# Performance work log

Hardware: AMD Instinct MI355X
Metric: run time of the kernel (lower is better)

## Reference

```python
import jax, jax.numpy as jnp
import numpy as np

N_BASIS = 128   # n_atom_basis F
N_INT   = 3     # n_interactions
N_RBF   = 20
CUTOFF  = 5.0
MAX_Z   = 100
EPS     = 1e-8
N_ATOMS = 25000
N_EDGES = 200000


def setup_inputs() -> dict:
    key = jax.random.key(0)
    ks = jax.random.split(key, 16)
    F = N_BASIS
    s = 0.02
    z     = jax.random.randint(ks[0], (N_ATOMS,), 1, MAX_Z)
    pos   = jax.random.uniform(ks[1], (N_ATOMS, 3), dtype=jnp.float32) * 2.0  # small box -> inside cutoff
    idx_i = jax.random.randint(ks[2], (N_EDGES,), 0, N_ATOMS)
    idx_j = jax.random.randint(ks[3], (N_EDGES,), 0, N_ATOMS)
    emb   = jax.random.normal(ks[4], (MAX_Z, F), dtype=jnp.float32) * s
    fW    = jax.random.normal(ks[5], (N_RBF, 3 * F * N_INT), dtype=jnp.float32) * s
    fb    = jnp.zeros((3 * F * N_INT,), jnp.float32)
    iW1   = jax.random.normal(ks[6], (N_INT, F, F), dtype=jnp.float32) * s
    ib1   = jnp.zeros((N_INT, F), jnp.float32)
    iW2   = jax.random.normal(ks[7], (N_INT, F, 3 * F), dtype=jnp.float32) * s
    ib2   = jnp.zeros((N_INT, 3 * F), jnp.float32)
    mWmix = jax.random.normal(ks[8], (N_INT, F, 2 * F), dtype=jnp.float32) * s
    mW1   = jax.random.normal(ks[9], (N_INT, 2 * F, F), dtype=jnp.float32) * s
    mb1   = jnp.zeros((N_INT, F), jnp.float32)
    mW2   = jax.random.normal(ks[10], (N_INT, F, 3 * F), dtype=jnp.float32) * s
    mb2   = jnp.zeros((N_INT, 3 * F), jnp.float32)
    return dict(z=z, pos=pos, idx_i=idx_i, idx_j=idx_j, emb=emb, fW=fW, fb=fb,
                iW1=iW1, ib1=ib1, iW2=iW2, ib2=ib2,
                mWmix=mWmix, mW1=mW1, mb1=mb1, mW2=mW2, mb2=mb2)


def reference(z, pos, idx_i, idx_j, emb, fW, fb, iW1, ib1, iW2, ib2,
              mWmix, mW1, mb1, mW2, mb2):
    F = N_BASIS
    n_atoms = z.shape[0]
    # geometry
    r_ij = pos[idx_j] - pos[idx_i]                                  # [E,3]
    r_ij = jnp.where(jnp.abs(r_ij) < 1e-6, 1e-6, r_ij)
    d_ij = jnp.linalg.norm(r_ij, axis=1, keepdims=True)             # [E,1]
    dir_ij = r_ij / d_ij                                            # [E,3]
    # Gaussian radial basis
    offsets = jnp.linspace(0.0, CUTOFF, N_RBF)
    width = offsets[1] - offsets[0]
    coeff = -0.5 / (width * width)
    phi = jnp.exp(coeff * (d_ij[..., None] - offsets) ** 2)         # [E,1,n_rbf]
    # cosine cutoff
    fcut = 0.5 * (jnp.cos(jnp.pi * d_ij / CUTOFF) + 1.0) * (d_ij < CUTOFF)  # [E,1]
    filters = (phi @ fW + fb) * fcut[..., None]                     # [E,1,3F*I]
    filter_list = jnp.split(filters, N_INT, axis=-1)                # each [E,1,3F]
    # initial atom features
    q = emb[z][:, None, :]                                          # [N,1,F]
    mu = jnp.zeros((n_atoms, 3, F), q.dtype)                        # [N,3,F]
    for t in range(N_INT):
        # --- interaction (gather - filter-multiply - scatter-add) ---
        x = jax.nn.silu(q @ iW1[t] + ib1[t]) @ iW2[t] + ib2[t]      # [N,1,3F]
        xj = x[idx_j]                                               # [E,1,3F]
        muj = mu[idx_j]                                             # [E,3,F]
        x = filter_list[t] * xj                                     # [E,1,3F]
        dq, dmuR, dmumu = jnp.split(x, 3, axis=-1)                  # [E,1,F] each
        dq = jax.ops.segment_sum(dq, idx_i, num_segments=n_atoms)   # [N,1,F]
        dmu = dmuR * dir_ij[..., None] + dmumu * muj                # [E,3,F]
        dmu = jax.ops.segment_sum(dmu, idx_i, num_segments=n_atoms) # [N,3,F]
        q = q + dq
        mu = mu + dmu
        # --- mixing (intra-atomic) ---
        mu_mix = mu @ mWmix[t]                                      # [N,3,2F]
        mu_V, mu_W = jnp.split(mu_mix, 2, axis=-1)                  # [N,3,F]
        mu_Vn = jnp.sqrt(jnp.sum(mu_V ** 2, axis=-2, keepdims=True) + EPS)  # [N,1,F]
        ctx = jnp.concatenate([q, mu_Vn], axis=-1)                  # [N,1,2F]
        x = jax.nn.silu(ctx @ mW1[t] + mb1[t]) @ mW2[t] + mb2[t]    # [N,1,3F]
        dq_intra, dmu_intra, dqmu_intra = jnp.split(x, 3, axis=-1)
        dmu_intra = dmu_intra * mu_W                                # [N,3,F]
        dqmu_intra = dqmu_intra * jnp.sum(mu_V * mu_W, axis=1, keepdims=True)
        q = q + dq_intra + dqmu_intra
        mu = mu + dmu_intra
    return q.squeeze(1), mu
```

## Files before the change

kernel.cpp:

```cpp
#include <hip/hip_runtime.h>
#include <hip/hip_bf16.h>

#define F 128
#define F3 384
#define NRBF 20
#define NITER 3
#define KP 24

typedef __hip_bfloat16 bf16;
typedef __bf16 bfrag __attribute__((ext_vector_type(8)));
typedef float f32x4 __attribute__((ext_vector_type(4)));

__device__ __forceinline__ float b2f(bf16 v) { return __bfloat162float(v); }
__device__ __forceinline__ bf16 f2b(float v) { return __float2bfloat16(v); }
__device__ __forceinline__ bfrag ldb(const bf16* p) { return *(const bfrag*)p; }
__device__ __forceinline__ bfrag ldsb(const __bf16* p) { return *(const bfrag*)p; }
__device__ __forceinline__ bfrag cvtf(const float* p) {
    bfrag r;
#pragma unroll
    for (int j = 0; j < 8; ++j) r[j] = (__bf16)p[j];
    return r;
}

__global__ void detect_kernel(const unsigned short* __restrict__ raw, int n_u16,
                              int* __restrict__ flag) {
    int i = blockIdx.x * blockDim.x + threadIdx.x;
    int bad = 0;
    for (int k = i; k < n_u16; k += blockDim.x * gridDim.x) {
        unsigned e = (raw[k] >> 7) & 0xFFu;
        if (e >= 140u) bad = 1;
    }
    if (bad) atomicOr(flag, 1);
}

struct CvtArgs {
    const void* src[13];
    float* dst[13];
    int end[14];
};
__global__ void cvt_all_kernel(CvtArgs a, const int* __restrict__ flag, int total) {
    int idx = blockIdx.x * blockDim.x + threadIdx.x;
    if (idx >= total) return;
    int s = 0;
    while (idx >= a.end[s + 1]) ++s;
    int local = idx - a.end[s];
    float v = (*flag) ? ((const float*)a.src[s])[local]
                      : b2f(((const bf16*)a.src[s])[local]);
    a.dst[s][local] = v;
}

struct TpArgs {
    const float* src[5];
    bf16* dst[5];
    int K[5];
    int Nn[5];
    int end[6];
};
__global__ void tpose_all_kernel(TpArgs a, int total) {
    int idx = blockIdx.x * blockDim.x + threadIdx.x;
    if (idx >= total) return;
    int s = 0;
    while (idx >= a.end[s + 1]) ++s;
    int local = idx - a.end[s];
    int K = a.K[s], Nn = a.Nn[s], slice = K * Nn;
    int t = local / slice, j = local - t * slice;
    int n = j / K, k = j - n * K;
    a.dst[s][local] = f2b(a.src[s][t * slice + k * Nn + n]);
}

__global__ void fwt_kernel(const float* __restrict__ fW, const float* __restrict__ fb,
                           float* __restrict__ dst, int total) {
    int idx = blockIdx.x * blockDim.x + threadIdx.x;
    if (idx >= total) return;
    int k = idx % KP, rest = idx / KP;
    int n = rest % F3, t = rest / F3;
    float v = (k < NRBF) ? fW[k * (F3 * NITER) + t * F3 + n]
                         : (k == NRBF ? fb[t * F3 + n] : 0.0f);
    dst[idx] = v;
}

__global__ void geom_kernel(const float* __restrict__ pos, const int* __restrict__ ii,
                            const int* __restrict__ jj, const int* __restrict__ rank,
                            float* __restrict__ phifc2, float* __restrict__ dir2,
                            int* __restrict__ jj2, int E) {
    int e = blockIdx.x * blockDim.x + threadIdx.x;
    if (e >= E) return;
    int i = ii[e], j = jj[e], l = rank[e];
    float r[3];
#pragma unroll
    for (int d = 0; d < 3; ++d) {
        float v = pos[j * 3 + d] - pos[i * 3 + d];
        if (fabsf(v) < 1e-6f) v = 1e-6f;
        r[d] = v;
    }
    float dd = sqrtf(r[0] * r[0] + r[1] * r[1] + r[2] * r[2]);
    float inv = 1.0f / dd;
    jj2[l] = j;
#pragma unroll
    for (int d = 0; d < 3; ++d) dir2[(size_t)l * 4 + d] = r[d] * inv;
    dir2[(size_t)l * 4 + 3] = 0.0f;
    const float CUT = 5.0f;
    const float PI = 3.14159265358979323846f;
    float fc = (dd < CUT) ? 0.5f * (cosf(PI * dd / CUT) + 1.0f) : 0.0f;
    const float width = CUT / (NRBF - 1);
    const float coeff = -0.5f / (width * width);
    float* pr = phifc2 + (size_t)l * KP;
#pragma unroll
    for (int k = 0; k < NRBF; ++k) {
        float diff = dd - (float)k * width;
        pr[k] = expf(coeff * diff * diff) * fc;
    }
    pr[NRBF] = fc;
    pr[NRBF + 1] = 0.0f;
    pr[NRBF + 2] = 0.0f;
    pr[NRBF + 3] = 0.0f;
}

__global__ void embed_kernel(const int* __restrict__ z, const float* __restrict__ emb,
                             float* __restrict__ q, int N) {
    int idx = blockIdx.x * blockDim.x + threadIdx.x;
    if (idx >= N * F) return;
    int n = idx >> 7, f = idx & 127;
    q[idx] = emb[z[n] * F + f];
}

__global__ void count_kernel(const int* __restrict__ ii, int* __restrict__ counts, int E) {
    int e = blockIdx.x * blockDim.x + threadIdx.x;
    if (e < E) atomicAdd(&counts[ii[e]], 1);
}

__global__ void scan_kernel(const int* __restrict__ counts, int* __restrict__ offs, int N) {
    __shared__ int cum[1024];
    int t = threadIdx.x;
    int chunk = (N + 1023) >> 10;
    int b = t * chunk;
    int e = b + chunk; if (e > N) e = N;
    int s = 0;
    for (int a = b; a < e; ++a) s += counts[a];
    cum[t] = s;
    __syncthreads();
    for (int o = 1; o < 1024; o <<= 1) {
        int u = (t >= o) ? cum[t - o] : 0;
        __syncthreads();
        cum[t] += u;
        __syncthreads();
    }
    int run = cum[t] - s;
    for (int a = b; a < e; ++a) { offs[a] = run; run += counts[a]; }
    if (t == 1023) offs[N] = cum[1023];
}

__global__ void fill_kernel(const int* __restrict__ ii, const int* __restrict__ offs,
                            int* __restrict__ cursor, int* __restrict__ rank, int E) {
    int e = blockIdx.x * blockDim.x + threadIdx.x;
    if (e >= E) return;
    int i = ii[e];
    int p = atomicAdd(&cursor[i], 1);
    rank[e] = offs[i] + p;
}

__global__ __launch_bounds__(256) void atom_x_mfma(
    const float* __restrict__ q, const bf16* __restrict__ W1T, const float* __restrict__ b1,
    const bf16* __restrict__ W2T, const float* __restrict__ b2, bf16* __restrict__ x, int N) {
    __shared__ __bf16 H[32][136];
    int tid = threadIdx.x;
    int w = tid >> 6, l = tid & 63;
    int lm = l & 15, q4 = l >> 4;
    int i0 = blockIdx.x * 32;
    f32x4 acc[2][2] = {};
    int r0 = min(i0 + lm, N - 1);
    int r1 = min(i0 + 16 + lm, N - 1);
    for (int kt = 0; kt < 4; ++kt) {
        int ko = kt * 32 + q4 * 8;
        bfrag a0 = cvtf(q + (size_t)r0 * F + ko);
        bfrag a1 = cvtf(q + (size_t)r1 * F + ko);
        bfrag b0 = ldb(W1T + (size_t)(w * 32 + lm) * F + ko);
        bfrag b1f = ldb(W1T + (size_t)(w * 32 + 16 + lm) * F + ko);
        acc[0][0] = __builtin_amdgcn_mfma_f32_16x16x32_bf16(a0, b0, acc[0][0], 0, 0, 0);
        acc[1][0] = __builtin_amdgcn_mfma_f32_16x16x32_bf16(a1, b0, acc[1][0], 0, 0, 0);
        acc[0][1] = __builtin_amdgcn_mfma_f32_16x16x32_bf16(a0, b1f, acc[0][1], 0, 0, 0);
        acc[1][1] = __builtin_amdgcn_mfma_f32_16x16x32_bf16(a1, b1f, acc[1][1], 0, 0, 0);
    }
#pragma unroll
    for (int nt = 0; nt < 2; ++nt) {
        int col = w * 32 + nt * 16 + lm;
        float bb = b1[col];
#pragma unroll
        for (int mt = 0; mt < 2; ++mt)
#pragma unroll
            for (int r = 0; r < 4; ++r) {
                float v = acc[mt][nt][r] + bb;
                H[mt * 16 + q4 * 4 + r][col] = (__bf16)(v / (1.0f + expf(-v)));
            }
    }
    __syncthreads();
#pragma unroll
    for (int j = 0; j < 6; ++j) {
        int n0 = w * 96 + j * 16;
        f32x4 c0 = {}, c1 = {};
        const bf16* bp = W2T + (size_t)(n0 + lm) * F;
        for (int kt = 0; kt < 4; ++kt) {
            int ko = kt * 32 + q4 * 8;
            bfrag a0 = ldsb(&H[lm][ko]);
            bfrag a1 = ldsb(&H[16 + lm][ko]);
            bfrag bf = ldb(bp + ko);
            c0 = __builtin_amdgcn_mfma_f32_16x16x32_bf16(a0, bf, c0, 0, 0, 0);
            c1 = __builtin_amdgcn_mfma_f32_16x16x32_bf16(a1, bf, c1, 0, 0, 0);
        }
        int col = n0 + lm;
        float bb = b2[col];
#pragma unroll
        for (int r = 0; r < 4; ++r) {
            int row0 = i0 + q4 * 4 + r;
            int row1 = row0 + 16;
            if (row0 < N) x[(size_t)row0 * F3 + col] = f2b(c0[r] + bb);
            if (row1 < N) x[(size_t)row1 * F3 + col] = f2b(c1[r] + bb);
        }
    }
}

__global__ __launch_bounds__(128, 2) void edge_gather_pin(
    float* __restrict__ q, const bf16* __restrict__ mu_in, const bf16* __restrict__ x,
    const float* __restrict__ phifc2, const float* __restrict__ dir2,
    const int* __restrict__ jj2, const float* __restrict__ fWTf,
    const int* __restrict__ offs, bf16* __restrict__ mu_out, int N) {
    int i = blockIdx.x;
    int f = threadIdx.x;
    float w0[21], w1[21], w2[21];
    {
        const f32x4* p0 = (const f32x4*)(fWTf + (size_t)f * KP);
        const f32x4* p1 = (const f32x4*)(fWTf + (size_t)(f + 128) * KP);
        const f32x4* p2 = (const f32x4*)(fWTf + (size_t)(f + 256) * KP);
#pragma unroll
        for (int k = 0; k < 6; ++k) {
            f32x4 t0 = p0[k], t1 = p1[k], t2 = p2[k];
#pragma unroll
            for (int r = 0; r < 4; ++r) {
                int kk = k * 4 + r;
                if (kk < 21) { w0[kk] = t0[r]; w1[kk] = t1[r]; w2[kk] = t2[r]; }
            }
        }
    }
#pragma unroll
    for (int k = 0; k < 21; ++k)
        asm volatile("" : "+v"(w0[k]), "+v"(w1[k]), "+v"(w2[k]));
    int beg = offs[i], end = offs[i + 1];
    float accq = 0.0f, am0 = 0.0f, am1 = 0.0f, am2 = 0.0f;
    for (int l = beg; l < end; ++l) {
        const f32x4* pr4 = (const f32x4*)(phifc2 + (size_t)l * KP);
        f32x4 p[6];
#pragma unroll
        for (int k = 0; k < 6; ++k) p[k] = pr4[k];
        float f0 = 0.0f, f1 = 0.0f, f2 = 0.0f;
#pragma unroll
        for (int k = 0; k < 21; ++k) {
            float ph = p[k >> 2][k & 3];
            f0 += ph * w0[k];
            f1 += ph * w1[k];
            f2 += ph * w2[k];
        }
        int j = jj2[l];
        f32x4 dv = *(const f32x4*)(dir2 + (size_t)l * 4);
        const bf16* xj = x + (size_t)j * F3;
        float dq = f0 * b2f(xj[f]);
        float dR = f1 * b2f(xj[f + 128]);
        float dM = f2 * b2f(xj[f + 256]);
        accq += dq;
        const bf16* muj = mu_in + (size_t)j * F3;
        am0 += dR * dv[0] + dM * b2f(muj[f]);
        am1 += dR * dv[1] + dM * b2f(muj[f + 128]);
        am2 += dR * dv[2] + dM * b2f(muj[f + 256]);
    }
    q[(size_t)i * F + f] += accq;
    size_t mb = (size_t)i * F3 + f;
    mu_out[mb]       = f2b(b2f(mu_in[mb]) + am0);
    mu_out[mb + 128] = f2b(b2f(mu_in[mb + 128]) + am1);
    mu_out[mb + 256] = f2b(b2f(mu_in[mb + 256]) + am2);
}

__global__ __launch_bounds__(256) void mix_mfma(
    float* __restrict__ q, bf16* __restrict__ mu,
    const bf16* __restrict__ WmixT, const bf16* __restrict__ W1T, const float* __restrict__ b1,
    const bf16* __restrict__ W2T, const float* __restrict__ b2, int N) {
    __shared__ __bf16 MM[48][264];
    __shared__ __bf16 CT[16][264];
    __shared__ __bf16 HM[16][136];
    __shared__ __bf16 Y[16][392];
    int tid = threadIdx.x;
    int w = tid >> 6, l = tid & 63;
    int lm = l & 15, q4 = l >> 4;
    int i0 = blockIdx.x * 16;
    int rowsM = N * 3;
    {
        f32x4 acc[3][4] = {};
        int mr[3];
#pragma unroll
        for (int mt = 0; mt < 3; ++mt) mr[mt] = min(i0 * 3 + mt * 16 + lm, rowsM - 1);
        for (int kt = 0; kt < 4; ++kt) {
            int ko = kt * 32 + q4 * 8;
            bfrag a[3], b[4];
#pragma unroll
            for (int mt = 0; mt < 3; ++mt) a[mt] = ldb(mu + (size_t)mr[mt] * F + ko);
#pragma unroll
            for (int nt = 0; nt < 4; ++nt)
                b[nt] = ldb(WmixT + (size_t)(w * 64 + nt * 16 + lm) * F + ko);
#pragma unroll
            for (int mt = 0; mt < 3; ++mt)
#pragma unroll
                for (int nt = 0; nt < 4; ++nt)
                    acc[mt][nt] = __builtin_amdgcn_mfma_f32_16x16x32_bf16(a[mt], b[nt], acc[mt][nt], 0, 0, 0);
        }
#pragma unroll
        for (int mt = 0; mt < 3; ++mt)
#pragma unroll
            for (int nt = 0; nt < 4; ++nt)
#pragma unroll
                for (int r = 0; r < 4; ++r)
                    MM[mt * 16 + q4 * 4 + r][w * 64 + nt * 16 + lm] = (__bf16)acc[mt][nt][r];
    }
    __syncthreads();
    for (int idx = tid; idx < 16 * F; idx += 256) {
        int a = idx >> 7, f = idx & 127;
        int i = min(i0 + a, N - 1);
        float v0 = (float)MM[a * 3 + 0][f];
        float v1 = (float)MM[a * 3 + 1][f];
        float v2 = (float)MM[a * 3 + 2][f];
        CT[a][f] = (__bf16)q[(size_t)i * F + f];
        CT[a][F + f] = (__bf16)sqrtf(v0 * v0 + v1 * v1 + v2 * v2 + 1e-8f);
    }
    __syncthreads();
    {
        f32x4 c[2] = {};
        for (int kt = 0; kt < 8; ++kt) {
            int ko = kt * 32 + q4 * 8;
            bfrag a = ldsb(&CT[lm][ko]);
#pragma unroll
            for (int nt = 0; nt < 2; ++nt) {
                bfrag b = ldb(W1T + (size_t)(w * 32 + nt * 16 + lm) * 256 + ko);
                c[nt] = __builtin_amdgcn_mfma_f32_16x16x32_bf16(a, b, c[nt], 0, 0, 0);
            }
        }
#pragma unroll
        for (int nt = 0; nt < 2; ++nt) {
            int col = w * 32 + nt * 16 + lm;
            float bb = b1[col];
#pragma unroll
            for (int r = 0; r < 4; ++r) {
                float v = c[nt][r] + bb;
                HM[q4 * 4 + r][col] = (__bf16)(v / (1.0f + expf(-v)));
            }
        }
    }
    __syncthreads();
#pragma unroll
    for (int j = 0; j < 6; ++j) {
        int n0 = w * 96 + j * 16;
        f32x4 c = {};
        const bf16* bp = W2T + (size_t)(n0 + lm) * F;
        for (int kt = 0; kt < 4; ++kt) {
            int ko = kt * 32 + q4 * 8;
            bfrag a = ldsb(&HM[lm][ko]);
            bfrag b = ldb(bp + ko);
            c = __builtin_amdgcn_mfma_f32_16x16x32_bf16(a, b, c, 0, 0, 0);
        }
        int col = n0 + lm;
        float bb = b2[col];
#pragma unroll
        for (int r = 0; r < 4; ++r)
            Y[q4 * 4 + r][col] = (__bf16)(c[r] + bb);
    }
    __syncthreads();
    for (int idx = tid; idx < 16 * F; idx += 256) {
        int a = idx >> 7, f = idx & 127;
        int i = i0 + a;
        if (i >= N) continue;
        float V0 = (float)MM[a * 3 + 0][f], W0 = (float)MM[a * 3 + 0][F + f];
        float V1 = (float)MM[a * 3 + 1][f], W1v = (float)MM[a * 3 + 1][F + f];
        float V2 = (float)MM[a * 3 + 2][f], W2v = (float)MM[a * 3 + 2][F + f];
        float s = V0 * W0 + V1 * W1v + V2 * W2v;
        float yq = (float)Y[a][f], ym = (float)Y[a][F + f], ys = (float)Y[a][2 * F + f];
        q[(size_t)i * F + f] += yq + ys * s;
        size_t mb = (size_t)i * F3 + f;
        mu[mb]       = f2b(b2f(mu[mb]) + ym * W0);
        mu[mb + 128] = f2b(b2f(mu[mb + 128]) + ym * W1v);
        mu[mb + 256] = f2b(b2f(mu[mb + 256]) + ym * W2v);
    }
}

__global__ void out_kernel(const float* __restrict__ q, const bf16* __restrict__ mu,
                           void* __restrict__ out, int N, const int* __restrict__ flag) {
    int idx = blockIdx.x * blockDim.x + threadIdx.x;
    int nq = N * F;
    int tot = nq + N * F3;
    if (idx >= tot) return;
    float v = (idx < nq) ? q[idx] : b2f(mu[idx - nq]);
    if (*flag) ((float*)out)[idx] = v;
    else       ((bf16*)out)[idx] = f2b(v);
}

extern "C" void kernel_launch(void* const* d_in, const int* in_sizes, int n_in,
                              void* d_out, int out_size, void* d_ws, size_t ws_size,
                              hipStream_t stream) {
    const int* z = (const int*)d_in[0];
    const int* idx_i = (const int*)d_in[2];
    const int* idx_j = (const int*)d_in[3];

    int N = in_sizes[0];
    int E = in_sizes[2];

    char* base = (char*)d_ws;
    size_t off = 0;
    auto alloc = [&](size_t bytes) -> void* {
        void* p = base + off;
        off += (bytes + 255) & ~(size_t)255;
        return p;
    };

    int* flag = (int*)alloc(4);
    float* pos_f = (float*)alloc((size_t)in_sizes[1] * 4);
    float* emb_f = (float*)alloc((size_t)in_sizes[4] * 4);
    float* fW_f = (float*)alloc((size_t)in_sizes[5] * 4);
    float* fb_f = (float*)alloc((size_t)in_sizes[6] * 4);
    float* iW1_f = (float*)alloc((size_t)in_sizes[7] * 4);
    float* ib1_f = (float*)alloc((size_t)in_sizes[8] * 4);
    float* iW2_f = (float*)alloc((size_t)in_sizes[9] * 4);
    float* ib2_f = (float*)alloc((size_t)in_sizes[10] * 4);
    float* mWmix_f = (float*)alloc((size_t)in_sizes[11] * 4);
    float* mW1_f = (float*)alloc((size_t)in_sizes[12] * 4);
    float* mb1_f = (float*)alloc((size_t)in_sizes[13] * 4);
    float* mW2_f = (float*)alloc((size_t)in_sizes[14] * 4);
    float* mb2_f = (float*)alloc((size_t)in_sizes[15] * 4);
    bf16* iW1T = (bf16*)alloc((size_t)NITER * F * F * 2);
    bf16* iW2T = (bf16*)alloc((size_t)NITER * F3 * F * 2);
    bf16* mWmixT = (bf16*)alloc((size_t)NITER * 2 * F * F * 2);
    bf16* mW1T = (bf16*)alloc((size_t)NITER * F * 2 * F * 2);
    bf16* mW2T = (bf16*)alloc((size_t)NITER * F3 * F * 2);
    float* fWTf = (float*)alloc((size_t)NITER * F3 * KP * 4);
    float* q = (float*)alloc((size_t)N * F * 4);
    bf16* mua = (bf16*)alloc((size_t)N * F3 * 2);
    bf16* mub = (bf16*)alloc((size_t)N * F3 * 2);
    bf16* xbuf = (bf16*)alloc((size_t)N * F3 * 2);
    float* phifc2 = (float*)alloc((size_t)(E + 16) * KP * 4);
    float* dir2 = (float*)alloc((size_t)(E + 16) * 4 * 4);
    int* jj2 = (int*)alloc((size_t)(E + 16) * 4);
    int* rank = (int*)alloc((size_t)E * 4);
    int* counts = (int*)alloc((size_t)N * 4);
    int* offs = (int*)alloc((size_t)(N + 1) * 4);

    hipMemsetAsync(flag, 0, 4, stream);
    detect_kernel<<<64, 256, 0, stream>>>((const unsigned short*)d_in[1], in_sizes[1], flag);

    {
        CvtArgs a;
        const int srcIdx[13] = {1, 4, 5, 6, 7, 8, 9, 10, 11, 12, 13, 14, 15};
        float* dsts[13] = {pos_f, emb_f, fW_f, fb_f, iW1_f, ib1_f, iW2_f, ib2_f,
                           mWmix_f, mW1_f, mb1_f, mW2_f, mb2_f};
        int cum = 0;
        a.end[0] = 0;
        for (int s = 0; s < 13; ++s) {
            a.src[s] = d_in[srcIdx[s]];
            a.dst[s] = dsts[s];
            cum += in_sizes[srcIdx[s]];
            a.end[s + 1] = cum;
        }
        cvt_all_kernel<<<(cum + 255) / 256, 256, 0, stream>>>(a, flag, cum);
    }

    {
        TpArgs a;
        const float* srcs[5] = {iW1_f, iW2_f, mWmix_f, mW1_f, mW2_f};
        bf16* dsts[5] = {iW1T, iW2T, mWmixT, mW1T, mW2T};
        int Ks[5] = {F, F, F, 2 * F, F};
        int Nns[5] = {F, F3, 2 * F, F, F3};
        int cum = 0;
        a.end[0] = 0;
        for (int s = 0; s < 5; ++s) {
            a.src[s] = srcs[s];
            a.dst[s] = dsts[s];
            a.K[s] = Ks[s];
            a.Nn[s] = Nns[s];
            cum += NITER * Ks[s] * Nns[s];
            a.end[s + 1] = cum;
        }
        tpose_all_kernel<<<(cum + 255) / 256, 256, 0, stream>>>(a, cum);
    }
    {
        int total = NITER * F3 * KP;
        fwt_kernel<<<(total + 255) / 256, 256, 0, stream>>>(fW_f, fb_f, fWTf, total);
    }

    hipMemsetAsync(counts, 0, (size_t)N * 4, stream);
    count_kernel<<<(E + 255) / 256, 256, 0, stream>>>(idx_i, counts, E);
    scan_kernel<<<1, 1024, 0, stream>>>(counts, offs, N);
    hipMemsetAsync(counts, 0, (size_t)N * 4, stream);
    fill_kernel<<<(E + 255) / 256, 256, 0, stream>>>(idx_i, offs, counts, rank, E);

    geom_kernel<<<(E + 255) / 256, 256, 0, stream>>>(pos_f, idx_i, idx_j, rank,
                                                     phifc2, dir2, jj2, E);
    embed_kernel<<<(N * F + 255) / 256, 256, 0, stream>>>(z, emb_f, q, N);
    hipMemsetAsync(mua, 0, (size_t)N * F3 * 2, stream);

    bf16* muin = mua;
    bf16* muout = mub;
    for (int t = 0; t < NITER; ++t) {
        atom_x_mfma<<<(N + 31) / 32, 256, 0, stream>>>(q, iW1T + (size_t)t * F * F, ib1_f + t * F,
                                                       iW2T + (size_t)t * F3 * F, ib2_f + t * F3,
                                                       xbuf, N);
        edge_gather_pin<<<N, 128, 0, stream>>>(q, muin, xbuf, phifc2, dir2, jj2,
                                               fWTf + (size_t)t * F3 * KP, offs, muout, N);
        mix_mfma<<<(N + 15) / 16, 256, 0, stream>>>(q, muout, mWmixT + (size_t)t * 2 * F * F,
                                                    mW1T + (size_t)t * F * 2 * F, mb1_f + t * F,
                                                    mW2T + (size_t)t * F3 * F, mb2_f + t * F3, N);
        bf16* tm = muin; muin = muout; muout = tm;
    }

    int tot = N * (F + F3);
    out_kernel<<<(tot + 255) / 256, 256, 0, stream>>>(q, muin, d_out, N, flag);
}
```

Measured before the change: 824.1 us.

## Persist edge-gather blocks over atom chunks, unroll edges, specialize first iteration

The edge gather kernel now launches a fixed grid of blocks, each looping over a contiguous chunk of atoms. This amortizes the per-block load of filter weights and reduces launch overhead. The edge loop is unrolled by two so gathers from independent edges can overlap. A template specialization for the first interaction skips the mu gathers and the third filter column, since mu starts at zero there. The cost is coarser load balancing across the fixed grid and extra code size.

Result: slower. 1.456 ms (+76.7%).

```diff
diff --git a/kernel.cpp b/kernel.cpp
--- a/kernel.cpp
+++ b/kernel.cpp
@@ -6,6 +6,7 @@
 #define NRBF 20
 #define NITER 3
 #define KP 24
+#define EGRID 2048
 
 typedef __hip_bfloat16 bf16;
 typedef __bf16 bfrag __attribute__((ext_vector_type(8)));
@@ -219,63 +220,163 @@
     }
 }
 
-__global__ __launch_bounds__(128, 2) void edge_gather_pin(
+template<int T0>
+__global__ __launch_bounds__(128, 2) void edge_gather_p(
     float* __restrict__ q, const bf16* __restrict__ mu_in, const bf16* __restrict__ x,
     const float* __restrict__ phifc2, const float* __restrict__ dir2,
     const int* __restrict__ jj2, const float* __restrict__ fWTf,
-    const int* __restrict__ offs, bf16* __restrict__ mu_out, int N) {
-    int i = blockIdx.x;
+    const int* __restrict__ offs, bf16* __restrict__ mu_out, int N, int chunk) {
+    int ibeg = blockIdx.x * chunk;
+    int iend = min(ibeg + chunk, N);
+    if (ibeg >= iend) return;
     int f = threadIdx.x;
     float w0[21], w1[21], w2[21];
     {
         const f32x4* p0 = (const f32x4*)(fWTf + (size_t)f * KP);
         const f32x4* p1 = (const f32x4*)(fWTf + (size_t)(f + 128) * KP);
-        const f32x4* p2 = (const f32x4*)(fWTf + (size_t)(f + 256) * KP);
 #pragma unroll
         for (int k = 0; k < 6; ++k) {
-            f32x4 t0 = p0[k], t1 = p1[k], t2 = p2[k];
+            f32x4 t0 = p0[k], t1 = p1[k];
 #pragma unroll
             for (int r = 0; r < 4; ++r) {
                 int kk = k * 4 + r;
-                if (kk < 21) { w0[kk] = t0[r]; w1[kk] = t1[r]; w2[kk] = t2[r]; }
-            }
-        }
-    }
-#pragma unroll
-    for (int k = 0; k < 21; ++k)
-        asm volatile("" : "+v"(w0[k]), "+v"(w1[k]), "+v"(w2[k]));
-    int beg = offs[i], end = offs[i + 1];
-    float accq = 0.0f, am0 = 0.0f, am1 = 0.0f, am2 = 0.0f;
-    for (int l = beg; l < end; ++l) {
-        const f32x4* pr4 = (const f32x4*)(phifc2 + (size_t)l * KP);
-        f32x4 p[6];
-#pragma unroll
-        for (int k = 0; k < 6; ++k) p[k] = pr4[k];
-        float f0 = 0.0f, f1 = 0.0f, f2 = 0.0f;
-#pragma unroll
-        for (int k = 0; k < 21; ++k) {
-            float ph = p[k >> 2][k & 3];
-            f0 += ph * w0[k];
-            f1 += ph * w1[k];
-            f2 += ph * w2[k];
-        }
-        int j = jj2[l];
-        f32x4 dv = *(const f32x4*)(dir2 + (size_t)l * 4);
-        const bf16* xj = x + (size_t)j * F3;
-        float dq = f0 * b2f(xj[f]);
-        float dR = f1 * b2f(xj[f + 128]);
-        float dM = f2 * b2f(xj[f + 256]);
-        accq += dq;
-        const bf16* muj = mu_in + (size_t)j * F3;
-        am0 += dR * dv[0] + dM * b2f(muj[f]);
-        am1 += dR * dv[1] + dM * b2f(muj[f + 128]);
-        am2 += dR * dv[2] + dM * b2f(muj[f + 256]);
-    }
-    q[(size_t)i * F + f] += accq;
-    size_t mb = (size_t)i * F3 + f;
-    mu_out[mb]       = f2b(b2f(mu_in[mb]) + am0);
-    mu_out[mb + 128] = f2b(b2f(mu_in[mb + 128]) + am1);
-    mu_out[mb + 256] = f2b(b2f(mu_in[mb + 256]) + am2);
+                if (kk < 21) { w0[kk] = t0[r]; w1[kk] = t1[r]; }
+            }
+        }
+        if constexpr (!T0) {
+            const f32x4* p2 = (const f32x4*)(fWTf + (size_t)(f + 256) * KP);
+#pragma unroll
+            for (int k = 0; k < 6; ++k) {
+                f32x4 t2 = p2[k];
+#pragma unroll
+                for (int r = 0; r < 4; ++r) {
+                    int kk = k * 4 + r;
+                    if (kk < 21) w2[kk] = t2[r];
+                }
+            }
+        }
+    }
+#pragma unroll
+    for (int k = 0; k < 21; ++k) {
+        asm volatile("" : "+v"(w0[k]), "+v"(w1[k]));
+        if constexpr (!T0) asm volatile("" : "+v"(w2[k]));
+    }
+    for (int i = ibeg; i < iend; ++i) {
+        int beg = offs[i], end = offs[i + 1];
+        float accq = 0.0f, am0 = 0.0f, am1 = 0.0f, am2 = 0.0f;
+        int l = beg;
+        for (; l + 1 < end; l += 2) {
+            int ja = jj2[l], jb = jj2[l + 1];
+            const bf16* xja = x + (size_t)ja * F3;
+            const bf16* xjb = x + (size_t)jb * F3;
+            float xa0 = b2f(xja[f]), xa1 = b2f(xja[f + 128]);
+            float xb0 = b2f(xjb[f]), xb1 = b2f(xjb[f + 128]);
+            float xa2, xb2, ma0, ma1, ma2, mb0, mb1, mb2;
+            if constexpr (!T0) {
+                xa2 = b2f(xja[f + 256]);
+                xb2 = b2f(xjb[f + 256]);
+                const bf16* mja = mu_in + (size_t)ja * F3;
+                const bf16* mjb = mu_in + (size_t)jb * F3;
+                ma0 = b2f(mja[f]); ma1 = b2f(mja[f + 128]); ma2 = b2f(mja[f + 256]);
+                mb0 = b2f(mjb[f]); mb1 = b2f(mjb[f + 128]); mb2 = b2f(mjb[f + 256]);
+            }
+            f32x4 dva = *(const f32x4*)(dir2 + (size_t)l * 4);
+            f32x4 dvb = *(const f32x4*)(dir2 + (size_t)(l + 1) * 4);
+            const f32x4* Pa = (const f32x4*)(phifc2 + (size_t)l * KP);
+            float f0a = 0.0f, f1a = 0.0f, f2a = 0.0f;
+#pragma unroll
+            for (int k = 0; k < 6; ++k) {
+                f32x4 ph4 = Pa[k];
+#pragma unroll
+                for (int r = 0; r < 4; ++r) {
+                    int kk = k * 4 + r;
+                    if (kk < 21) {
+                        float ph = ph4[r];
+                        f0a += ph * w0[kk];
+                        f1a += ph * w1[kk];
+                        if constexpr (!T0) f2a += ph * w2[kk];
+                    }
+                }
+            }
+            const f32x4* Pb = Pa + 6;
+            float f0b = 0.0f, f1b = 0.0f, f2b_ = 0.0f;
+#pragma unroll
+            for (int k = 0; k < 6; ++k) {
+                f32x4 ph4 = Pb[k];
+#pragma unroll
+                for (int r = 0; r < 4; ++r) {
+                    int kk = k * 4 + r;
+                    if (kk < 21) {
+                        float ph = ph4[r];
+                        f0b += ph * w0[kk];
+                        f1b += ph * w1[kk];
+                        if constexpr (!T0) f2b_ += ph * w2[kk];
+                    }
+                }
+            }
+            accq += f0a * xa0 + f0b * xb0;
+            float dRa = f1a * xa1, dRb = f1b * xb1;
+            am0 += dRa * dva[0] + dRb * dvb[0];
+            am1 += dRa * dva[1] + dRb * dvb[1];
+            am2 += dRa * dva[2] + dRb * dvb[2];
+            if constexpr (!T0) {
+                float dMa = f2a * xa2, dMb = f2b_ * xb2;
+                am0 += dMa * ma0 + dMb * mb0;
+                am1 += dMa * ma1 + dMb * mb1;
+                am2 += dMa * ma2 + dMb * mb2;
+            }
+        }
+        if (l < end) {
+            int ja = jj2[l];
+            const bf16* xja = x + (size_t)ja * F3;
+            float xa0 = b2f(xja[f]), xa1 = b2f(xja[f + 128]);
+            float xa2, ma0, ma1, ma2;
+            if constexpr (!T0) {
+                xa2 = b2f(xja[f + 256]);
+                const bf16* mja = mu_in + (size_t)ja * F3;
+                ma0 = b2f(mja[f]); ma1 = b2f(mja[f + 128]); ma2 = b2f(mja[f + 256]);
+            }
+            f32x4 dva = *(const f32x4*)(dir2 + (size_t)l * 4);
+            const f32x4* Pa = (const f32x4*)(phifc2 + (size_t)l * KP);
+            float f0a = 0.0f, f1a = 0.0f, f2a = 0.0f;
+#pragma unroll
+            for (int k = 0; k < 6; ++k) {
+                f32x4 ph4 = Pa[k];
+#pragma unroll
+                for (int r = 0; r < 4; ++r) {
+                    int kk = k * 4 + r;
+                    if (kk < 21) {
+                        float ph = ph4[r];
+                        f0a += ph * w0[kk];
+                        f1a += ph * w1[kk];
+                        if constexpr (!T0) f2a += ph * w2[kk];
+                    }
+                }
+            }
+            accq += f0a * xa0;
+            float dRa = f1a * xa1;
+            am0 += dRa * dva[0];
+            am1 += dRa * dva[1];
+            am2 += dRa * dva[2];
+            if constexpr (!T0) {
+                float dMa = f2a * xa2;
+                am0 += dMa * ma0;
+                am1 += dMa * ma1;
+                am2 += dMa * ma2;
+            }
+        }
+        q[(size_t)i * F + f] += accq;
+        size_t mb_ = (size_t)i * F3 + f;
+        if constexpr (T0) {
+            mu_out[mb_]       = f2b(am0);
+            mu_out[mb_ + 128] = f2b(am1);
+            mu_out[mb_ + 256] = f2b(am2);
+        } else {
+            mu_out[mb_]       = f2b(b2f(mu_in[mb_]) + am0);
+            mu_out[mb_ + 128] = f2b(b2f(mu_in[mb_ + 128]) + am1);
+            mu_out[mb_ + 256] = f2b(b2f(mu_in[mb_ + 256]) + am2);
+        }
+    }
 }
 
 __global__ __launch_bounds__(256) void mix_mfma(
@@ -500,14 +601,21 @@
     embed_kernel<<<(N * F + 255) / 256, 256, 0, stream>>>(z, emb_f, q, N);
     hipMemsetAsync(mua, 0, (size_t)N * F3 * 2, stream);
 
+    int chunk = (N + EGRID - 1) / EGRID;
     bf16* muin = mua;
     bf16* muout = mub;
     for (int t = 0; t < NITER; ++t) {
         atom_x_mfma<<<(N + 31) / 32, 256, 0, stream>>>(q, iW1T + (size_t)t * F * F, ib1_f + t * F,
                                                        iW2T + (size_t)t * F3 * F, ib2_f + t * F3,
                                                        xbuf, N);
-        edge_gather_pin<<<N, 128, 0, stream>>>(q, muin, xbuf, phifc2, dir2, jj2,
-                                               fWTf + (size_t)t * F3 * KP, offs, muout, N);
+        if (t == 0)
+            edge_gather_p<1><<<EGRID, 128, 0, stream>>>(q, muin, xbuf, phifc2, dir2, jj2,
+                                                        fWTf + (size_t)t * F3 * KP, offs, muout,
+                                                        N, chunk);
+        else
+            edge_gather_p<0><<<EGRID, 128, 0, stream>>>(q, muin, xbuf, phifc2, dir2, jj2,
+                                                        fWTf + (size_t)t * F3 * KP, offs, muout,
+                                                        N, chunk);
         mix_mfma<<<(N + 15) / 16, 256, 0, stream>>>(q, muout, mWmixT + (size_t)t * 2 * F * F,
                                                     mW1T + (size_t)t * F * 2 * F, mb1_f + t * F,
                                                     mW2T + (size_t)t * F3 * F, mb2_f + t * F3, N);
```

## Specialize first edge iteration for zero mu, pack neighbor index into dir

Applied to the files above, without the earlier changes.

Adds a templated edge-gather kernel whose first-iteration variant exploits mu starting at zero. It skips the third filter channel, the x/mu neighbor gathers for the mu-mu term, and the read of mu_in, and it drops the memset of the initial mu buffer. The neighbor index j is stored bit-cast in the unused fourth lane of dir2, which removes the separate jj2 array and one load per edge. Edge-stream loads are marked nontemporal to reduce cache pollution. The gains are confined to one of the three iterations plus the removed memset.

Result: faster. 772.6 us (-6.3%).

```diff
diff --git a/kernel.cpp b/kernel.cpp
--- a/kernel.cpp
+++ b/kernel.cpp
@@ -81,8 +81,7 @@
 
 __global__ void geom_kernel(const float* __restrict__ pos, const int* __restrict__ ii,
                             const int* __restrict__ jj, const int* __restrict__ rank,
-                            float* __restrict__ phifc2, float* __restrict__ dir2,
-                            int* __restrict__ jj2, int E) {
+                            float* __restrict__ phifc2, float* __restrict__ dir2, int E) {
     int e = blockIdx.x * blockDim.x + threadIdx.x;
     if (e >= E) return;
     int i = ii[e], j = jj[e], l = rank[e];
@@ -95,10 +94,9 @@
     }
     float dd = sqrtf(r[0] * r[0] + r[1] * r[1] + r[2] * r[2]);
     float inv = 1.0f / dd;
-    jj2[l] = j;
 #pragma unroll
     for (int d = 0; d < 3; ++d) dir2[(size_t)l * 4 + d] = r[d] * inv;
-    dir2[(size_t)l * 4 + 3] = 0.0f;
+    dir2[(size_t)l * 4 + 3] = __int_as_float(j);
     const float CUT = 5.0f;
     const float PI = 3.14159265358979323846f;
     float fc = (dd < CUT) ? 0.5f * (cosf(PI * dd / CUT) + 1.0f) : 0.0f;
@@ -219,10 +217,11 @@
     }
 }
 
-__global__ __launch_bounds__(128, 2) void edge_gather_pin(
+template<int T0>
+__global__ __launch_bounds__(128, 2) void edge_gather_t(
     float* __restrict__ q, const bf16* __restrict__ mu_in, const bf16* __restrict__ x,
     const float* __restrict__ phifc2, const float* __restrict__ dir2,
-    const int* __restrict__ jj2, const float* __restrict__ fWTf,
+    const float* __restrict__ fWTf,
     const int* __restrict__ offs, bf16* __restrict__ mu_out, int N) {
     int i = blockIdx.x;
     int f = threadIdx.x;
@@ -230,52 +229,77 @@
     {
         const f32x4* p0 = (const f32x4*)(fWTf + (size_t)f * KP);
         const f32x4* p1 = (const f32x4*)(fWTf + (size_t)(f + 128) * KP);
-        const f32x4* p2 = (const f32x4*)(fWTf + (size_t)(f + 256) * KP);
 #pragma unroll
         for (int k = 0; k < 6; ++k) {
-            f32x4 t0 = p0[k], t1 = p1[k], t2 = p2[k];
+            f32x4 t0 = p0[k], t1 = p1[k];
 #pragma unroll
             for (int r = 0; r < 4; ++r) {
                 int kk = k * 4 + r;
-                if (kk < 21) { w0[kk] = t0[r]; w1[kk] = t1[r]; w2[kk] = t2[r]; }
+                if (kk < 21) { w0[kk] = t0[r]; w1[kk] = t1[r]; }
             }
         }
-    }
-#pragma unroll
-    for (int k = 0; k < 21; ++k)
-        asm volatile("" : "+v"(w0[k]), "+v"(w1[k]), "+v"(w2[k]));
+        if constexpr (!T0) {
+            const f32x4* p2 = (const f32x4*)(fWTf + (size_t)(f + 256) * KP);
+#pragma unroll
+            for (int k = 0; k < 6; ++k) {
+                f32x4 t2 = p2[k];
+#pragma unroll
+                for (int r = 0; r < 4; ++r) {
+                    int kk = k * 4 + r;
+                    if (kk < 21) w2[kk] = t2[r];
+                }
+            }
+        }
+    }
+#pragma unroll
+    for (int k = 0; k < 21; ++k) {
+        asm volatile("" : "+v"(w0[k]), "+v"(w1[k]));
+        if constexpr (!T0) asm volatile("" : "+v"(w2[k]));
+    }
     int beg = offs[i], end = offs[i + 1];
     float accq = 0.0f, am0 = 0.0f, am1 = 0.0f, am2 = 0.0f;
     for (int l = beg; l < end; ++l) {
         const f32x4* pr4 = (const f32x4*)(phifc2 + (size_t)l * KP);
         f32x4 p[6];
 #pragma unroll
-        for (int k = 0; k < 6; ++k) p[k] = pr4[k];
-        float f0 = 0.0f, f1 = 0.0f, f2 = 0.0f;
+        for (int k = 0; k < 6; ++k) p[k] = __builtin_nontemporal_load(pr4 + k);
+        float fl0 = 0.0f, fl1 = 0.0f, fl2 = 0.0f;
 #pragma unroll
         for (int k = 0; k < 21; ++k) {
             float ph = p[k >> 2][k & 3];
-            f0 += ph * w0[k];
-            f1 += ph * w1[k];
-            f2 += ph * w2[k];
-        }
-        int j = jj2[l];
-        f32x4 dv = *(const f32x4*)(dir2 + (size_t)l * 4);
+            fl0 += ph * w0[k];
+            fl1 += ph * w1[k];
+            if constexpr (!T0) fl2 += ph * w2[k];
+        }
+        f32x4 dv = __builtin_nontemporal_load((const f32x4*)(dir2 + (size_t)l * 4));
+        int j = __float_as_int(dv[3]);
         const bf16* xj = x + (size_t)j * F3;
-        float dq = f0 * b2f(xj[f]);
-        float dR = f1 * b2f(xj[f + 128]);
-        float dM = f2 * b2f(xj[f + 256]);
+        float dq = fl0 * b2f(xj[f]);
+        float dR = fl1 * b2f(xj[f + 128]);
         accq += dq;
-        const bf16* muj = mu_in + (size_t)j * F3;
-        am0 += dR * dv[0] + dM * b2f(muj[f]);
-        am1 += dR * dv[1] + dM * b2f(muj[f + 128]);
-        am2 += dR * dv[2] + dM * b2f(muj[f + 256]);
+        if constexpr (!T0) {
+            float dM = fl2 * b2f(xj[f + 256]);
+            const bf16* muj = mu_in + (size_t)j * F3;
+            am0 += dR * dv[0] + dM * b2f(muj[f]);
+            am1 += dR * dv[1] + dM * b2f(muj[f + 128]);
+            am2 += dR * dv[2] + dM * b2f(muj[f + 256]);
+        } else {
+            am0 += dR * dv[0];
+            am1 += dR * dv[1];
+            am2 += dR * dv[2];
+        }
     }
     q[(size_t)i * F + f] += accq;
     size_t mb = (size_t)i * F3 + f;
-    mu_out[mb]       = f2b(b2f(mu_in[mb]) + am0);
-    mu_out[mb + 128] = f2b(b2f(mu_in[mb + 128]) + am1);
-    mu_out[mb + 256] = f2b(b2f(mu_in[mb + 256]) + am2);
+    if constexpr (T0) {
+        mu_out[mb]       = f2b(am0);
+        mu_out[mb + 128] = f2b(am1);
+        mu_out[mb + 256] = f2b(am2);
+    } else {
+        mu_out[mb]       = f2b(b2f(mu_in[mb]) + am0);
+        mu_out[mb + 128] = f2b(b2f(mu_in[mb + 128]) + am1);
+        mu_out[mb + 256] = f2b(b2f(mu_in[mb + 256]) + am2);
+    }
 }
 
 __global__ __launch_bounds__(256) void mix_mfma(
@@ -442,7 +466,6 @@
     bf16* xbuf = (bf16*)alloc((size_t)N * F3 * 2);
     float* phifc2 = (float*)alloc((size_t)(E + 16) * KP * 4);
     float* dir2 = (float*)alloc((size_t)(E + 16) * 4 * 4);
-    int* jj2 = (int*)alloc((size_t)(E + 16) * 4);
     int* rank = (int*)alloc((size_t)E * 4);
     int* counts = (int*)alloc((size_t)N * 4);
     int* offs = (int*)alloc((size_t)(N + 1) * 4);
@@ -496,9 +519,8 @@
     fill_kernel<<<(E + 255) / 256, 256, 0, stream>>>(idx_i, offs, counts, rank, E);
 
     geom_kernel<<<(E + 255) / 256, 256, 0, stream>>>(pos_f, idx_i, idx_j, rank,
-                                                     phifc2, dir2, jj2, E);
+                                                     phifc2, dir2, E);
     embed_kernel<<<(N * F + 255) / 256, 256, 0, stream>>>(z, emb_f, q, N);
-    hipMemsetAsync(mua, 0, (size_t)N * F3 * 2, stream);
 
     bf16* muin = mua;
     bf16* muout = mub;
@@ -506,8 +528,12 @@
         atom_x_mfma<<<(N + 31) / 32, 256, 0, stream>>>(q, iW1T + (size_t)t * F * F, ib1_f + t * F,
                                                        iW2T + (size_t)t * F3 * F, ib2_f + t * F3,
                                                        xbuf, N);
-        edge_gather_pin<<<N, 128, 0, stream>>>(q, muin, xbuf, phifc2, dir2, jj2,
-                                               fWTf + (size_t)t * F3 * KP, offs, muout, N);
+        if (t == 0)
+            edge_gather_t<1><<<N, 128, 0, stream>>>(q, muin, xbuf, phifc2, dir2,
+                                                    fWTf + (size_t)t * F3 * KP, offs, muout, N);
+        else
+            edge_gather_t<0><<<N, 128, 0, stream>>>(q, muin, xbuf, phifc2, dir2,
+                                                    fWTf + (size_t)t * F3 * KP, offs, muout, N);
         mix_mfma<<<(N + 15) / 16, 256, 0, stream>>>(q, muout, mWmixT + (size_t)t * 2 * F * F,
                                                     mW1T + (size_t)t * F * 2 * F, mb1_f + t * F,
                                                     mW2T + (size_t)t * F3 * F, mb2_f + t * F3, N);
```
